# Optimization experiments

Measured on AMD Instinct MI355X. Metric: run time of the kernel, lower is better.

The kernel has to match this reference:

```python
import jax, jax.numpy as jnp
import numpy as np

N = 50000      # nodes
E = 600000     # edges
D = 128        # num_features == hidden_dim
H = 1          # heads (only runnable config of this module)
C = 128        # per-head channels
L = 2          # num_layers
G = 64         # graphs in batch
NC = 10        # num_classes


def setup_inputs() -> dict:
    key = jax.random.key(0)
    ks = jax.random.split(key, 12)
    s = 1.0 / np.sqrt(D)
    inp = {
        "x": jax.random.normal(ks[0], (N, D), jnp.float32),
        "edge_index": jax.random.randint(ks[1], (2, E), 0, N),
        "batch": jnp.sort(jax.random.randint(ks[2], (N,), 0, G)),
        # per-layer TransformerConv params (stacked over layers)
        "Wq": jax.random.normal(ks[3], (L, D, H * C), jnp.float32) * s,
        "bq": jax.random.normal(ks[4], (L, H * C), jnp.float32) * 0.01,
        "Wk": jax.random.normal(ks[5], (L, D, H * C), jnp.float32) * s,
        "bk": jax.random.normal(ks[6], (L, H * C), jnp.float32) * 0.01,
        "Wv": jax.random.normal(ks[7], (L, D, H * C), jnp.float32) * s,
        "bv": jax.random.normal(ks[8], (L, H * C), jnp.float32) * 0.01,
        "Ws": jax.random.normal(ks[9], (L, D, H * C), jnp.float32) * s,  # lin_skip (root weight)
        "bs": jax.random.normal(ks[10], (L, H * C), jnp.float32) * 0.01,
        "W_fc": jax.random.normal(ks[11], (H * C, NC), jnp.float32) * (1.0 / np.sqrt(H * C)),
        "b_fc": jnp.zeros((NC,), jnp.float32),
    }
    return inp


def _transformer_conv(x, src, dst, wq, bq, wk, bk, wv, bv, ws, bs):
    n = x.shape[0]
    q = (x @ wq + bq).reshape(n, H, C)
    k = (x @ wk + bk).reshape(n, H, C)
    v = (x @ wv + bv).reshape(n, H, C)
    # edge-wise gather: query from dst (x_i), key/value from src (x_j)
    score = (q[dst] * k[src]).sum(-1) / jnp.sqrt(jnp.float32(C))  # [E, H]
    # segment softmax over incoming edges of each dst node
    m = jax.ops.segment_max(score, dst, num_segments=n)           # [N, H]
    ex = jnp.exp(score - m[dst])
    den = jax.ops.segment_sum(ex, dst, num_segments=n)
    alpha = ex / den[dst]                                         # [E, H]
    agg = jax.ops.segment_sum(alpha[..., None] * v[src], dst, num_segments=n)
    return agg.reshape(n, H * C) + x @ ws + bs                    # concat heads + skip


def reference(x, edge_index, batch, Wq, bq, Wk, bk, Wv, bv, Ws, bs, W_fc, b_fc):
    src, dst = edge_index[0], edge_index[1]
    h = x
    for l in range(L):
        h = jax.nn.relu(_transformer_conv(h, src, dst, Wq[l], bq[l], Wk[l], bk[l],
                                          Wv[l], bv[l], Ws[l], bs[l]))
    # global mean pool per graph
    sums = jax.ops.segment_sum(h, batch, num_segments=G)
    cnts = jax.ops.segment_sum(jnp.ones((h.shape[0],), h.dtype), batch, num_segments=G)
    pooled = sums / jnp.maximum(cnts, 1.0)[:, None]
    logits = pooled @ W_fc + b_fc
    return jax.nn.log_softmax(logits, axis=1)
```

## Files before the change

### kernel.cpp

```cpp
#include <hip/hip_runtime.h>
#include <math.h>

#define NN 50000
#define EE 600000
#define DD 128
#define GG 64
#define NCLS 10
#define PCHUNK 128
#define NTILE (NN / 16)
#define NBUK 196
#define BSTRIDE 4096
#define EPB ((EE + 255) / 256)

typedef __attribute__((ext_vector_type(8))) __bf16 bf16x8;
typedef __attribute__((ext_vector_type(8))) unsigned short u16x8;
typedef __attribute__((ext_vector_type(4))) float f32x4;
typedef __attribute__((ext_vector_type(2))) float f32x2;

__device__ __forceinline__ unsigned short f2bf(float f) {
    unsigned int u = __float_as_uint(f);
    u += 0x7fff + ((u >> 16) & 1);
    return (unsigned short)(u >> 16);
}

__device__ __forceinline__ float bf2f(unsigned short h) {
    return __uint_as_float(((unsigned int)h) << 16);
}

__device__ __forceinline__ float lo16(unsigned int u) { return __uint_as_float(u << 16); }
__device__ __forceinline__ float hi16(unsigned int u) { return __uint_as_float(u & 0xffff0000u); }


__global__ __launch_bounds__(256) void prep_kernel(
    const float* __restrict__ wq, const float* __restrict__ wk,
    const float* __restrict__ wv, const float* __restrict__ ws,
    const float* __restrict__ x, unsigned short* __restrict__ xb,
    unsigned short* __restrict__ wt,
    int* __restrict__ bucketcnt, float* __restrict__ gsum) {
    int tid = blockIdx.x * 256 + threadIdx.x;
    int TOT = gridDim.x * 256;
    if (tid < 256) bucketcnt[tid] = 0;
    for (int i = tid; i < GG * DD + GG; i += TOT) gsum[i] = 0.f;
    for (int i = tid; i < 2 * 4 * 16384; i += TOT) {
        int k = i & 127;
        int n = (i >> 7) & 127;
        int lm = i >> 14;
        int l = lm >> 2, m = lm & 3;
        const float* w = (m == 0) ? wq : (m == 1) ? wk : (m == 2) ? wv : ws;
        wt[i] = f2bf(w[l * 16384 + k * 128 + n]);
    }
    for (int i = tid; i < NN * DD / 8; i += TOT) {
        const float* px = x + (size_t)i * 8;
        float4 f0 = *(const float4*)px;
        float4 f1 = *(const float4*)(px + 4);
        u16x8 o;
        o[0] = f2bf(f0.x); o[1] = f2bf(f0.y); o[2] = f2bf(f0.z); o[3] = f2bf(f0.w);
        o[4] = f2bf(f1.x); o[5] = f2bf(f1.y); o[6] = f2bf(f1.z); o[7] = f2bf(f1.w);
        *(u16x8*)(xb + (size_t)i * 8) = o;
    }
}


__global__ __launch_bounds__(1024) void bucket_kernel(
    const int* __restrict__ src, const int* __restrict__ dst,
    int* __restrict__ bucketcnt, int2* __restrict__ bedge) {
    __shared__ int hist[256];
    __shared__ int base[256];
    int t = threadIdx.x;
    if (t < 256) hist[t] = 0;
    __syncthreads();
    int e0 = blockIdx.x * EPB;
    int eend = min(e0 + EPB, EE);

    int b0 = -1, b1 = -1, b2 = -1;
    int sl0 = 0, sl1 = 0, sl2 = 0;
    int s0 = 0, s1 = 0, s2 = 0, d0 = 0, d1 = 0, d2 = 0;
    int i = e0 + t;
    if (i < eend) { d0 = dst[i]; s0 = src[i]; b0 = d0 >> 8; sl0 = atomicAdd(&hist[b0], 1); }
    i += 1024;
    if (i < eend) { d1 = dst[i]; s1 = src[i]; b1 = d1 >> 8; sl1 = atomicAdd(&hist[b1], 1); }
    i += 1024;
    if (i < eend) { d2 = dst[i]; s2 = src[i]; b2 = d2 >> 8; sl2 = atomicAdd(&hist[b2], 1); }
    __syncthreads();

    if (t < 256) {
        int h = hist[t];
        base[t] = h ? atomicAdd(&bucketcnt[t], h) : 0;
    }
    __syncthreads();

    if (b0 >= 0) bedge[b0 * BSTRIDE + base[b0] + sl0] = make_int2(s0, d0);
    if (b1 >= 0) bedge[b1 * BSTRIDE + base[b1] + sl1] = make_int2(s1, d1);
    if (b2 >= 0) bedge[b2 * BSTRIDE + base[b2] + sl2] = make_int2(s2, d2);
}


__global__ __launch_bounds__(1024) void bsort_kernel(
    const int* __restrict__ bucketcnt, const int2* __restrict__ bedge,
    int* __restrict__ indptr, int* __restrict__ esrc) {
    __shared__ int buf[256];
    __shared__ int cur[256];
    int b = blockIdx.x;
    int t = threadIdx.x;

    if (t < 256) buf[t] = (t < NBUK) ? bucketcnt[t] : 0;
    __syncthreads();
    if (t < 64) {
        int carry = 0;
        #pragma unroll
        for (int c = 0; c < 4; ++c) {
            int v = buf[c * 64 + t];
            int x = v;
            #pragma unroll
            for (int off = 1; off < 64; off <<= 1) {
                int y = __shfl_up(x, off);
                if (t >= off) x += y;
            }
            cur[c * 64 + t] = carry + x - v;
            carry += __shfl(x, 63);
        }
    }
    __syncthreads();
    int count = buf[b];
    int bstart = cur[b];
    int node0 = b << 8;
    int nn = min(256, NN - node0);
    if (b == 0 && t == 0) indptr[NN] = EE;
    __syncthreads();
    if (t < 256) buf[t] = 0;
    __syncthreads();

    const int2* be = bedge + (size_t)b * BSTRIDE;
    for (int i2 = t; i2 < count; i2 += 1024)
        atomicAdd(&buf[be[i2].y - node0], 1);
    __syncthreads();

    if (t < 64) {
        int carry = 0;
        #pragma unroll
        for (int c = 0; c < 4; ++c) {
            int v = buf[c * 64 + t];
            int x = v;
            #pragma unroll
            for (int off = 1; off < 64; off <<= 1) {
                int y = __shfl_up(x, off);
                if (t >= off) x += y;
            }
            cur[c * 64 + t] = carry + x - v;
            carry += __shfl(x, 63);
        }
    }
    __syncthreads();
    if (t < nn) indptr[node0 + t] = bstart + cur[t];
    __syncthreads();

    for (int i2 = t; i2 < count; i2 += 1024) {
        int2 e = be[i2];
        int slot = atomicAdd(&cur[e.y - node0], 1);
        esrc[bstart + slot] = e.x;
    }
}


__global__ __launch_bounds__(256, 4) void gemm_mfma(
    const unsigned short* __restrict__ xin,
    const unsigned short* __restrict__ wt,
    const float* __restrict__ bq, const float* __restrict__ bk,
    const float* __restrict__ bv, const float* __restrict__ bs,
    unsigned short* __restrict__ qb, unsigned short* __restrict__ sb,
    unsigned char* __restrict__ kv8) {
    __shared__ __align__(16) unsigned short stg[2][16][136];

    int wid = threadIdx.x >> 6;
    int lane = threadIdx.x & 63;
    int typeB = blockIdx.x & 1;
    int mi = wid >> 1;
    int ch = wid & 1;
    int mat = typeB ? (mi ? 2 : 1) : (mi ? 3 : 0);
    int wseq = blockIdx.x >> 1;
    int lr = lane & 15, quad = lane >> 4;

    const unsigned short* wm_ = wt + mat * 16384;
    const float* bias = (mat == 0) ? bq : (mat == 1) ? bk : (mat == 2) ? bv : bs;

    bf16x8 bfr[4][4];
    #pragma unroll
    for (int ks = 0; ks < 4; ++ks)
        #pragma unroll
        for (int tn = 0; tn < 4; ++tn)
            bfr[ks][tn] = *(const bf16x8*)(wm_ + (ch * 64 + tn * 16 + lr) * 128
                                               + ks * 32 + quad * 8);
    float bcol[4];
    #pragma unroll
    for (int tn = 0; tn < 4; ++tn) bcol[tn] = bias[ch * 64 + tn * 16 + lr];

    int t = threadIdx.x;
    int rr = t >> 4;
    int cj = t & 15;

    for (int tile = wseq; tile < NTILE; tile += 256) {
        int row0 = tile * 16;
        bf16x8 af[4];
        #pragma unroll
        for (int ks = 0; ks < 4; ++ks)
            af[ks] = *(const bf16x8*)(xin + (size_t)(row0 + lr) * DD + ks * 32 + quad * 8);

        f32x4 acc[4];
        #pragma unroll
        for (int tn = 0; tn < 4; ++tn) acc[tn] = (f32x4){0.f, 0.f, 0.f, 0.f};
        #pragma unroll
        for (int ks = 0; ks < 4; ++ks)
            #pragma unroll
            for (int tn = 0; tn < 4; ++tn)
                acc[tn] = __builtin_amdgcn_mfma_f32_16x16x32_bf16(
                    af[ks], bfr[ks][tn], acc[tn], 0, 0, 0);

        #pragma unroll
        for (int tn = 0; tn < 4; ++tn)
            #pragma unroll
            for (int r = 0; r < 4; ++r)
                stg[mi][quad * 4 + r][ch * 64 + tn * 16 + lr] = f2bf(acc[tn][r] + bcol[tn]);
        __syncthreads();

        if (!typeB) {
            uint4 vq = *(const uint4*)&stg[0][rr][cj * 8];
            *(uint4*)(qb + (size_t)(row0 + rr) * 128 + cj * 8) = vq;
            uint4 vs = *(const uint4*)&stg[1][rr][cj * 8];
            *(uint4*)(sb + (size_t)(row0 + rr) * 128 + cj * 8) = vs;
        } else {
            uint4 kk = *(const uint4*)&stg[0][rr][cj * 8];
            uint4 vv = *(const uint4*)&stg[1][rr][cj * 8];
            unsigned int w0 = __builtin_amdgcn_cvt_pk_fp8_f32(lo16(kk.x), hi16(kk.x), 0, false);
            w0 = __builtin_amdgcn_cvt_pk_fp8_f32(lo16(kk.y), hi16(kk.y), w0, true);
            unsigned int w1 = __builtin_amdgcn_cvt_pk_fp8_f32(lo16(kk.z), hi16(kk.z), 0, false);
            w1 = __builtin_amdgcn_cvt_pk_fp8_f32(lo16(kk.w), hi16(kk.w), w1, true);
            unsigned int w2 = __builtin_amdgcn_cvt_pk_fp8_f32(lo16(vv.x), hi16(vv.x), 0, false);
            w2 = __builtin_amdgcn_cvt_pk_fp8_f32(lo16(vv.y), hi16(vv.y), w2, true);
            unsigned int w3 = __builtin_amdgcn_cvt_pk_fp8_f32(lo16(vv.z), hi16(vv.z), 0, false);
            w3 = __builtin_amdgcn_cvt_pk_fp8_f32(lo16(vv.w), hi16(vv.w), w3, true);
            *(uint4*)(kv8 + (size_t)(row0 + rr) * 256 + cj * 16) = make_uint4(w0, w1, w2, w3);
        }
        __syncthreads();
    }
}


__global__ __launch_bounds__(256) void attn_kernel(
    const unsigned short* __restrict__ qb, const unsigned char* __restrict__ kv8,
    const unsigned short* __restrict__ sb,
    const int* __restrict__ indptr, const int* __restrict__ esrc,
    unsigned short* __restrict__ hout, int n) {
    int node = (int)((blockIdx.x * blockDim.x + threadIdx.x) >> 6);
    int lane = threadIdx.x & 63;
    if (node >= n) return;
    int g = lane >> 4, j = lane & 15;

    u16x8 q8 = *(const u16x8*)(qb + (size_t)node * DD + j * 8);
    float qf[8];
    #pragma unroll
    for (int c = 0; c < 8; ++c) qf[c] = bf2f(q8[c]);

    int beg = indptr[node], end = indptr[node + 1];

    float m = -3.0e38f, den = 0.f;
    float acc[8];
    #pragma unroll
    for (int c = 0; c < 8; ++c) acc[c] = 0.f;

    int e = beg + g;
    if (e < end) {
        int sidx = esrc[e];
        int en = e + 4;
        int sn = (en < end) ? esrc[en] : 0;
        uint4 kv = *(const uint4*)(kv8 + (size_t)sidx * 256 + j * 16);
        for (;;) {
            bool haven = en < end;
            int en2 = en + 4;
            int sn2 = (en2 < end) ? esrc[en2] : 0;
            uint4 kvn;
            if (haven)
                kvn = *(const uint4*)(kv8 + (size_t)sn * 256 + j * 16);
            f32x2 k01 = __builtin_amdgcn_cvt_pk_f32_fp8(kv.x, false);
            f32x2 k23 = __builtin_amdgcn_cvt_pk_f32_fp8(kv.x, true);
            f32x2 k45 = __builtin_amdgcn_cvt_pk_f32_fp8(kv.y, false);
            f32x2 k67 = __builtin_amdgcn_cvt_pk_f32_fp8(kv.y, true);
            float p_;
            p_ = qf[0] * k01.x;
            p_ = fmaf(qf[1], k01.y, p_);
            p_ = fmaf(qf[2], k23.x, p_);
            p_ = fmaf(qf[3], k23.y, p_);
            p_ = fmaf(qf[4], k45.x, p_);
            p_ = fmaf(qf[5], k45.y, p_);
            p_ = fmaf(qf[6], k67.x, p_);
            p_ = fmaf(qf[7], k67.y, p_);
            p_ += __shfl_xor(p_, 8);
            p_ += __shfl_xor(p_, 4);
            p_ += __shfl_xor(p_, 2);
            p_ += __shfl_xor(p_, 1);
            float score = p_ * 0.088388347648318447f;
            float mn = fmaxf(m, score);
            float scale = __expf(m - mn);
            float pe = __expf(score - mn);
            den = den * scale + pe;
            f32x2 v01 = __builtin_amdgcn_cvt_pk_f32_fp8(kv.z, false);
            f32x2 v23 = __builtin_amdgcn_cvt_pk_f32_fp8(kv.z, true);
            f32x2 v45 = __builtin_amdgcn_cvt_pk_f32_fp8(kv.w, false);
            f32x2 v67 = __builtin_amdgcn_cvt_pk_f32_fp8(kv.w, true);
            acc[0] = fmaf(acc[0], scale, pe * v01.x);
            acc[1] = fmaf(acc[1], scale, pe * v01.y);
            acc[2] = fmaf(acc[2], scale, pe * v23.x);
            acc[3] = fmaf(acc[3], scale, pe * v23.y);
            acc[4] = fmaf(acc[4], scale, pe * v45.x);
            acc[5] = fmaf(acc[5], scale, pe * v45.y);
            acc[6] = fmaf(acc[6], scale, pe * v67.x);
            acc[7] = fmaf(acc[7], scale, pe * v67.y);
            m = mn;
            if (!haven) break;
            en = en2; sn = sn2; kv = kvn;
        }
    }

    float mo = __shfl_xor(m, 16);
    float m2 = fmaxf(m, mo);
    mo = __shfl_xor(m2, 32);
    float mf = fmaxf(m2, mo);
    float sc = __expf(m - mf);
    den *= sc;
    den += __shfl_xor(den, 16);
    den += __shfl_xor(den, 32);
    #pragma unroll
    for (int c = 0; c < 8; ++c) {
        float a = acc[c] * sc;
        a += __shfl_xor(a, 16);
        a += __shfl_xor(a, 32);
        acc[c] = a;
    }
    float inv = den > 0.f ? 1.0f / den : 0.f;
    if (g == 0) {
        u16x8 s8 = *(const u16x8*)(sb + (size_t)node * DD + j * 8);
        u16x8 o8;
        #pragma unroll
        for (int c = 0; c < 8; ++c)
            o8[c] = f2bf(fmaxf(fmaf(acc[c], inv, bf2f(s8[c])), 0.f));
        *(u16x8*)(hout + (size_t)node * DD + j * 8) = o8;
    }
}


__global__ __launch_bounds__(128) void pool_kernel(const unsigned short* __restrict__ h,
                                                   const int* __restrict__ batch,
                                                   float* __restrict__ gsum,
                                                   float* __restrict__ gcnt, int n) {
    __shared__ int bsh[PCHUNK];
    int t = threadIdx.x;
    int node0 = blockIdx.x * PCHUNK;
    int nnodes = min(PCHUNK, n - node0);
    if (t < nnodes) bsh[t] = batch[node0 + t];
    __syncthreads();

    int cur = bsh[0];
    float acc = 0.f;
    int cnt = 0;
    for (int j = 0; j < nnodes; ++j) {
        int g = bsh[j];
        float val = bf2f(h[(size_t)(node0 + j) * DD + t]);
        if (g != cur) {
            atomicAdd(&gsum[cur * DD + t], acc);
            if (t == 0) atomicAdd(&gcnt[cur], (float)cnt);
            acc = 0.f; cnt = 0; cur = g;
        }
        acc += val; ++cnt;
    }
    if (cnt > 0) {
        atomicAdd(&gsum[cur * DD + t], acc);
        if (t == 0) atomicAdd(&gcnt[cur], (float)cnt);
    }
}


__global__ __launch_bounds__(64) void head_kernel(
    const float* __restrict__ gsum, const float* __restrict__ gcnt,
    const float* __restrict__ wfc, const float* __restrict__ bfc,
    float* __restrict__ out) {
    int g = blockIdx.x;
    int lane = threadIdx.x;
    float cnt = fmaxf(gcnt[g], 1.0f);
    float inv = 1.0f / cnt;
    float p0 = gsum[g * DD + lane] * inv;
    float p1 = gsum[g * DD + lane + 64] * inv;
    __shared__ float logits[NCLS];
    for (int c = 0; c < NCLS; ++c) {
        float partial = p0 * wfc[lane * NCLS + c] + p1 * wfc[(lane + 64) * NCLS + c];
        partial += __shfl_xor(partial, 32);
        partial += __shfl_xor(partial, 16);
        partial += __shfl_xor(partial, 8);
        partial += __shfl_xor(partial, 4);
        partial += __shfl_xor(partial, 2);
        partial += __shfl_xor(partial, 1);
        if (lane == 0) logits[c] = partial + bfc[c];
    }
    __syncthreads();
    if (lane == 0) {
        float mx = logits[0];
        for (int c = 1; c < NCLS; ++c) mx = fmaxf(mx, logits[c]);
        float sum = 0.f;
        for (int c = 0; c < NCLS; ++c) sum += expf(logits[c] - mx);
        float lse = mx + logf(sum);
        for (int c = 0; c < NCLS; ++c) out[g * NCLS + c] = logits[c] - lse;
    }
}


extern "C" void kernel_launch(void* const* d_in, const int* in_sizes, int n_in,
                              void* d_out, int out_size, void* d_ws, size_t ws_size,
                              hipStream_t stream) {
    const float* x     = (const float*)d_in[0];
    const int*   ei    = (const int*)d_in[1];
    const int*   batch = (const int*)d_in[2];
    const float* Wq = (const float*)d_in[3];
    const float* bq = (const float*)d_in[4];
    const float* Wk = (const float*)d_in[5];
    const float* bk = (const float*)d_in[6];
    const float* Wv = (const float*)d_in[7];
    const float* bv = (const float*)d_in[8];
    const float* Ws = (const float*)d_in[9];
    const float* bs = (const float*)d_in[10];
    const float* Wfc = (const float*)d_in[11];
    const float* bfc = (const float*)d_in[12];
    float* out = (float*)d_out;

    const size_t ND = (size_t)NN * DD;
    unsigned short* hbuf = (unsigned short*)d_ws;
    unsigned short* qb  = hbuf + ND;
    unsigned short* sb  = qb + ND;
    unsigned short* wt  = sb + ND;
    unsigned char*  kv8 = (unsigned char*)(wt + 2 * 4 * 16384);
    unsigned short* xb  = (unsigned short*)(kv8 + (size_t)NN * 256);
    int* bucketcnt = (int*)(xb + ND);
    int* indptr    = bucketcnt + 256;
    int* esrc      = indptr + NN + 1;
    int2* bedge    = (int2*)(esrc + EE);
    float* gsum = (float*)(bedge + NBUK * BSTRIDE);
    float* gcnt = gsum + GG * DD;

    const int* src = ei;
    const int* dst = ei + EE;

    prep_kernel<<<512, 256, 0, stream>>>(Wq, Wk, Wv, Ws, x, xb, wt, bucketcnt, gsum);
    bucket_kernel<<<256, 1024, 0, stream>>>(src, dst, bucketcnt, bedge);
    bsort_kernel<<<NBUK, 1024, 0, stream>>>(bucketcnt, bedge, indptr, esrc);

    for (int l = 0; l < 2; ++l) {
        size_t bo = (size_t)l * DD;
        const unsigned short* wtl = wt + (size_t)l * 4 * 16384;
        gemm_mfma<<<512, 256, 0, stream>>>(
            (l == 0) ? xb : hbuf, wtl, bq + bo, bk + bo, bv + bo, bs + bo,
            qb, sb, kv8);
        attn_kernel<<<(NN + 3) / 4, 256, 0, stream>>>(
            qb, kv8, sb, indptr, esrc, hbuf, NN);
    }

    pool_kernel<<<(NN + PCHUNK - 1) / PCHUNK, 128, 0, stream>>>(hbuf, batch, gsum, gcnt, NN);
    head_kernel<<<GG, 64, 0, stream>>>(gsum, gcnt, Wfc, bfc, out);
}
```

Baseline: 258.4 us.

## Double-buffer GEMM input loads, lighten barriers, unroll pool loads, halve pool chunk

The GEMM kernel now prefetches the next tile's A fragments into a second register buffer while the current tile is computed. It also replaces __syncthreads with an LDS-only waitcnt plus s_barrier, so outstanding global loads can stay in flight. Launch bounds drop to 2 waves per EU to make room for the extra registers. The pool kernel batches four row loads before doing the segment logic and uses smaller chunks to get more blocks, at the cost of more atomics.

```diff
diff --git a/kernel.cpp b/kernel.cpp
--- a/kernel.cpp
+++ b/kernel.cpp
@@ -6,7 +6,7 @@
 #define DD 128
 #define GG 64
 #define NCLS 10
-#define PCHUNK 128
+#define PCHUNK 64
 #define NTILE (NN / 16)
 #define NBUK 196
 #define BSTRIDE 4096
@@ -16,6 +16,9 @@
 typedef __attribute__((ext_vector_type(8))) unsigned short u16x8;
 typedef __attribute__((ext_vector_type(4))) float f32x4;
 typedef __attribute__((ext_vector_type(2))) float f32x2;
+
+#define LGKM_FENCE() asm volatile("s_waitcnt lgkmcnt(0)" ::: "memory")
+#define SCHED_FENCE() __builtin_amdgcn_sched_barrier(0)
 
 __device__ __forceinline__ unsigned short f2bf(float f) {
     unsigned int u = __float_as_uint(f);
@@ -162,7 +165,7 @@
 }
 
 
-__global__ __launch_bounds__(256, 4) void gemm_mfma(
+__global__ __launch_bounds__(256, 2) void gemm_mfma(
     const unsigned short* __restrict__ xin,
     const unsigned short* __restrict__ wt,
     const float* __restrict__ bq, const float* __restrict__ bk,
@@ -198,13 +201,17 @@
     int rr = t >> 4;
     int cj = t & 15;
 
-    for (int tile = wseq; tile < NTILE; tile += 256) {
+    bf16x8 bufA[4], bufB[4];
+
+    auto load_t = [&](bf16x8 (&b)[4], int tl) {
+        const unsigned short* p = xin + (size_t)(tl * 16 + lr) * DD + quad * 8;
+        #pragma unroll
+        for (int ks = 0; ks < 4; ++ks)
+            b[ks] = *(const bf16x8*)(p + ks * 32);
+    };
+
+    auto compute_store = [&](bf16x8 (&b)[4], int tile) {
         int row0 = tile * 16;
-        bf16x8 af[4];
-        #pragma unroll
-        for (int ks = 0; ks < 4; ++ks)
-            af[ks] = *(const bf16x8*)(xin + (size_t)(row0 + lr) * DD + ks * 32 + quad * 8);
-
         f32x4 acc[4];
         #pragma unroll
         for (int tn = 0; tn < 4; ++tn) acc[tn] = (f32x4){0.f, 0.f, 0.f, 0.f};
@@ -213,14 +220,17 @@
             #pragma unroll
             for (int tn = 0; tn < 4; ++tn)
                 acc[tn] = __builtin_amdgcn_mfma_f32_16x16x32_bf16(
-                    af[ks], bfr[ks][tn], acc[tn], 0, 0, 0);
+                    b[ks], bfr[ks][tn], acc[tn], 0, 0, 0);
 
         #pragma unroll
         for (int tn = 0; tn < 4; ++tn)
             #pragma unroll
             for (int r = 0; r < 4; ++r)
                 stg[mi][quad * 4 + r][ch * 64 + tn * 16 + lr] = f2bf(acc[tn][r] + bcol[tn]);
-        __syncthreads();
+        SCHED_FENCE();
+        LGKM_FENCE();
+        __builtin_amdgcn_s_barrier();
+        SCHED_FENCE();
 
         if (!typeB) {
             uint4 vq = *(const uint4*)&stg[0][rr][cj * 8];
@@ -240,7 +250,25 @@
             w3 = __builtin_amdgcn_cvt_pk_fp8_f32(lo16(vv.w), hi16(vv.w), w3, true);
             *(uint4*)(kv8 + (size_t)(row0 + rr) * 256 + cj * 16) = make_uint4(w0, w1, w2, w3);
         }
-        __syncthreads();
+        SCHED_FENCE();
+        LGKM_FENCE();
+        __builtin_amdgcn_s_barrier();
+        SCHED_FENCE();
+    };
+
+    int tile = wseq;
+    load_t(bufA, tile);
+    for (;;) {
+        int t2 = tile + 256;
+        if (t2 < NTILE) load_t(bufB, t2);
+        compute_store(bufA, tile);
+        if (t2 >= NTILE) break;
+        tile = t2;
+        int t3 = tile + 256;
+        if (t3 < NTILE) load_t(bufA, t3);
+        compute_store(bufB, tile);
+        if (t3 >= NTILE) break;
+        tile = t3;
     }
 }
 
@@ -361,15 +389,24 @@
     int cur = bsh[0];
     float acc = 0.f;
     int cnt = 0;
-    for (int j = 0; j < nnodes; ++j) {
-        int g = bsh[j];
-        float val = bf2f(h[(size_t)(node0 + j) * DD + t]);
-        if (g != cur) {
-            atomicAdd(&gsum[cur * DD + t], acc);
-            if (t == 0) atomicAdd(&gcnt[cur], (float)cnt);
-            acc = 0.f; cnt = 0; cur = g;
+    for (int j0 = 0; j0 < nnodes; j0 += 4) {
+        int jm = min(4, nnodes - j0);
+        float v[4];
+        #pragma unroll
+        for (int u = 0; u < 4; ++u)
+            v[u] = (u < jm) ? bf2f(h[(size_t)(node0 + j0 + u) * DD + t]) : 0.f;
+        #pragma unroll
+        for (int u = 0; u < 4; ++u) {
+            if (u < jm) {
+                int g = bsh[j0 + u];
+                if (g != cur) {
+                    atomicAdd(&gsum[cur * DD + t], acc);
+                    if (t == 0) atomicAdd(&gcnt[cur], (float)cnt);
+                    acc = 0.f; cnt = 0; cur = g;
+                }
+                acc += v[u]; ++cnt;
+            }
         }
-        acc += val; ++cnt;
     }
     if (cnt > 0) {
         atomicAdd(&gsum[cur * DD + t], acc);
```

Measured after the change: 251.9 us. 1.03x faster.
